# Kernel optimization log

Measured on AMD Instinct MI355X. Metric: run time of the kernel, lower is better.

Reference implementation:

```python
import jax, jax.numpy as jnp
import numpy as np
import math

N_NODES, CHANNELS, N_ELEM, N_FEAT = 4096, 128, 10, 128
LS_IN = [0, 1, 2]          # input irreps per channel: 0e+1o+2e -> dim 9
L_OUT = [0, 1]             # keep_irrep_out = {0e, 1o}
L12_MAX = 3                # cap on intermediate coupling
SLICES = {0: (0, 1), 1: (1, 4), 2: (4, 9)}
PATHS1 = [l for l in L_OUT if l in LS_IN]
PATHS2 = [(l1, l2, lo) for l1 in LS_IN for l2 in LS_IN for lo in L_OUT if abs(l1 - l2) <= lo <= l1 + l2]
T12_KEYS = [(l1, l2, l12) for l1 in LS_IN for l2 in LS_IN for l12 in range(abs(l1 - l2), min(l1 + l2, L12_MAX) + 1)]
PATHS3 = [(k, l3, lo) for k in T12_KEYS for l3 in LS_IN for lo in L_OUT if abs(k[2] - l3) <= lo <= k[2] + l3]

def _su2_cg(j1, m1, j2, m2, j3, m3):
    if m3 != m1 + m2:
        return 0.0
    f = math.factorial
    vmin = max(-j1 + j2 + m3, -j1 + m1, 0)
    vmax = min(j2 + j3 + m1, j3 - j1 + j2, j3 + m3)
    C = math.sqrt((2 * j3 + 1) * f(j3 + j1 - j2) * f(j3 - j1 + j2) * f(j1 + j2 - j3) * f(j3 + m3) * f(j3 - m3)
                  / (f(j1 + j2 + j3 + 1) * f(j1 - m1) * f(j1 + m1) * f(j2 - m2) * f(j2 + m2)))
    S = 0.0
    for v in range(vmin, vmax + 1):
        S += (-1) ** (v + j2 + m2) * f(j2 + j3 + m1 - v) * f(j1 - m1 + v) / (
            f(v) * f(j3 - j1 + j2 - v) * f(j3 + m3 - v) * f(v + j1 - j2 - m3))
    return C * S

def _c2r(l):
    # change of basis real -> complex spherical harmonics (e3nn convention)
    q = np.zeros((2 * l + 1, 2 * l + 1), dtype=np.complex128)
    for m in range(-l, 0):
        q[l + m, l + abs(m)] = 1.0 / math.sqrt(2)
        q[l + m, l - abs(m)] = -1j / math.sqrt(2)
    q[l, l] = 1.0
    for m in range(1, l + 1):
        q[l + m, l + abs(m)] = (-1) ** m / math.sqrt(2)
        q[l + m, l - abs(m)] = 1j * (-1) ** m / math.sqrt(2)
    return (-1j) ** l * q

_CG = {}
def real_cg(l1, l2, l3):
    key = (l1, l2, l3)
    if key not in _CG:
        Cc = np.zeros((2 * l1 + 1, 2 * l2 + 1, 2 * l3 + 1), dtype=np.complex128)
        for i, m1 in enumerate(range(-l1, l1 + 1)):
            for j, m2 in enumerate(range(-l2, l2 + 1)):
                for k, m3 in enumerate(range(-l3, l3 + 1)):
                    Cc[i, j, k] = _su2_cg(l1, m1, l2, m2, l3, m3)
        R = np.einsum('ij,kl,mn,ikn->jlm', _c2r(l1), _c2r(l2), np.conj(_c2r(l3).T), Cc)
        _CG[key] = np.real(R).astype(np.float32)
    return _CG[key]

def setup_inputs():
    key = jax.random.key(0)
    k = jax.random.split(key, 8)
    node_feats = jax.random.normal(k[0], (N_NODES, CHANNELS, 9), dtype=jnp.float32)
    species = jax.random.randint(k[1], (N_NODES,), 0, N_ELEM)
    w1 = jax.random.normal(k[2], (N_ELEM, len(PATHS1), CHANNELS), dtype=jnp.float32) / math.sqrt(len(PATHS1))
    w2 = jax.random.normal(k[3], (N_ELEM, len(PATHS2), CHANNELS), dtype=jnp.float32) / math.sqrt(len(PATHS2))
    w3 = jax.random.normal(k[4], (N_ELEM, len(PATHS3), CHANNELS), dtype=jnp.float32) / math.sqrt(len(PATHS3))
    lin_w0 = jax.random.normal(k[5], (CHANNELS, N_FEAT), dtype=jnp.float32)
    lin_w1 = jax.random.normal(k[6], (CHANNELS, N_FEAT), dtype=jnp.float32)
    return {"node_feats": node_feats, "w1": w1, "w2": w2, "w3": w3,
            "lin_w0": lin_w0, "lin_w1": lin_w1, "species": species}

def reference(node_feats, w1, w2, w3, lin_w0, lin_w1, species):
    n, c = node_feats.shape[:2]
    attrs = jax.nn.one_hot(species, N_ELEM, dtype=node_feats.dtype)
    A = {l: node_feats[..., SLICES[l][0]:SLICES[l][1]] for l in LS_IN}
    # element-dependent path weights per node
    w1n = jnp.einsum('ne,epc->npc', attrs, w1)
    w2n = jnp.einsum('ne,epc->npc', attrs, w2)
    w3n = jnp.einsum('ne,epc->npc', attrs, w3)
    B = {lo: jnp.zeros((n, c, 2 * lo + 1), node_feats.dtype) for lo in L_OUT}
    # correlation order 1
    for p, lo in enumerate(PATHS1):
        B[lo] = B[lo] + w1n[:, p, :, None] * A[lo]
    for p, (l1, l2, lo) in enumerate(PATHS2):
        cg = jnp.asarray(real_cg(l1, l2, lo))
        t = jnp.einsum('ijk,nci,ncj->nck', cg, A[l1], A[l2])
        B[lo] = B[lo] + w2n[:, p, :, None] * t
    T12 = {}
    for kk in T12_KEYS:
        l1, l2, l12 = kk
        T12[kk] = jnp.einsum('ijk,nci,ncj->nck', jnp.asarray(real_cg(l1, l2, l12)), A[l1], A[l2])
    for p, (kk, l3, lo) in enumerate(PATHS3):
        cg = jnp.asarray(real_cg(kk[2], l3, lo))
        t = jnp.einsum('ijk,nci,ncj->nck', cg, T12[kk], A[l3])
        B[lo] = B[lo] + w3n[:, p, :, None] * t
    # equivariant Linear: mix channel axis into num_features per output irrep
    s = 1.0 / math.sqrt(c)
    out0 = jnp.einsum('ncm,cf->nfm', B[0], lin_w0) * s
    out1 = jnp.einsum('ncm,cf->nfm', B[1], lin_w1) * s
    return jnp.concatenate([out0, out1], axis=-1)  # [N, F, 1+3]
```

## Files before the change

### kernel.cpp

```cpp
#include <hip/hip_runtime.h>
#include <utility>


#define NN 4096
#define NC 128
#define NE 10
#define LTN 8

typedef float v2f __attribute__((ext_vector_type(2)));

__device__ __forceinline__ v2f ld2(const float* p) {
  return *reinterpret_cast<const v2f*>(p);
}
__device__ __forceinline__ v2f cfma(float c, v2f x, v2f a) {
  v2f cc = {c, c};
  return __builtin_elementwise_fma(cc, x, a);
}
__device__ __forceinline__ v2f vfma(v2f w, v2f x, v2f a) {
  return __builtin_elementwise_fma(w, x, a);
}

template<typename F, int... Is>
__device__ __forceinline__ void sfor_impl(F&& f, std::integer_sequence<int, Is...>) {
  (f(std::integral_constant<int, Is>{}), ...);
}
template<int N, typename F>
__device__ __forceinline__ void sfor(F&& f) {
  sfor_impl((F&&)f, std::make_integer_sequence<int, N>{});
}

constexpr int T_L1c[19]  = {0,0,0,1,1,1,1,1,1,1,2,2,2,2,2,2,2,2,3};
constexpr int T_L2c[19]  = {0,1,2,0,1,1,1,2,2,2,0,1,1,1,2,2,2,2,2};
constexpr int T_L3c[19]  = {0,1,2,1,0,1,2,1,2,3,2,1,2,3,0,1,2,3,1};
constexpr int T_OFFc[19] = {0,1,10,35,44,53,80,125,170,245,350,375,420,495,600,625,700,825,1000};
constexpr int AOFFc[3]   = {0,1,4};

constexpr int P2U_L1c[7]  = {0,0,1,1,1,2,2};
constexpr int P2U_L2c[7]  = {0,1,1,1,2,2,2};
constexpr int P2U_LOc[7]  = {0,1,0,1,1,0,1};
constexpr int P2U_TBLc[7] = {0,1,4,5,7,14,15};
constexpr int P2U_WAc[7]  = {0,1,3,4,5,7,8};
constexpr int P2U_WBc[7]  = {-1,2,-1,-1,6,-1,-1};

constexpr int K_L1c[18]  = {0,0,0,1,1,1,1,1,1,1,2,2,2,2,2,2,2,2};
constexpr int K_L2c[18]  = {0,1,2,0,1,1,1,2,2,2,0,1,1,1,2,2,2,2};
constexpr int K_L12c[18] = {0,1,2,1,0,1,2,1,2,3,2,1,2,3,0,1,2,3};

constexpr int   TT_CANONc[18] = {0,1,2,1,4,5,6,7,8,9,2,7,8,9,14,15,16,17};
constexpr float TT_SGNc[18]   = {1,1,1,1,1,1,1,1,1,1,1,1,-1,1,1,1,1,1};
constexpr int CANONc[13] = {0,1,2,4,5,6,7,8,9,14,15,16,17};
constexpr int CONS2c[13] = {-1,3,10,-1,-1,-1,11,12,13,-1,-1,-1,-1};

constexpr int P3_STARTc[19] = {0,2,6,9,13,15,19,22,26,29,30,33,37,40,41,43,47,50,51};
constexpr int P3_L3c[51] = {
  0,1,  0,1,1,2,  1,2,2,  0,1,1,2,  0,1,  0,1,1,2,  1,2,2,  0,1,1,2,  1,2,2,
  2,  1,2,2,  0,1,1,2,  1,2,2,  2,  0,1,  0,1,1,2,  1,2,2,  2 };
constexpr int P3_LOc[51] = {
  0,1,  1,0,1,1,  1,0,1,  1,0,1,1,  0,1,  1,0,1,1,  1,0,1,  1,0,1,1,  1,0,1,
  1,  1,0,1,  1,0,1,1,  1,0,1,  1,  0,1,  1,0,1,1,  1,0,1,  1 };
constexpr int P3_TBLc[51] = {
  0,1,  3,4,5,7,  11,14,15,  3,4,5,7,  0,1,  3,4,5,7,  11,14,15,  3,4,5,7,
  11,14,15,  18,  11,14,15,  3,4,5,7,  11,14,15,  18,  0,1,  3,4,5,7,
  11,14,15,  18 };

constexpr double cfact(int n) { double r = 1.0; for (int i = 2; i <= n; ++i) r *= i; return r; }
constexpr double csqrt(double x) {
  if (x <= 0.0) return 0.0;
  double r = x > 1.0 ? x : 1.0;
  for (int i = 0; i < 64; ++i) r = 0.5 * (r + x / r);
  return r;
}
constexpr double su2cg(int j1, int m1, int j2, int m2, int j3, int m3) {
  if (m3 != m1 + m2) return 0.0;
  int vmin = -j1 + j2 + m3; if (-j1 + m1 > vmin) vmin = -j1 + m1; if (vmin < 0) vmin = 0;
  int vmax = j2 + j3 + m1; if (j3 - j1 + j2 < vmax) vmax = j3 - j1 + j2; if (j3 + m3 < vmax) vmax = j3 + m3;
  double C = csqrt((2.0 * j3 + 1.0)
                   * cfact(j3 + j1 - j2) * cfact(j3 - j1 + j2) * cfact(j1 + j2 - j3)
                   * cfact(j3 + m3) * cfact(j3 - m3)
                   / (cfact(j1 + j2 + j3 + 1) * cfact(j1 - m1) * cfact(j1 + m1)
                      * cfact(j2 - m2) * cfact(j2 + m2)));
  double S = 0.0;
  for (int v = vmin; v <= vmax; ++v) {
    double sgn = ((v + j2 + m2) & 1) ? -1.0 : 1.0;
    S += sgn * cfact(j2 + j3 + m1 - v) * cfact(j1 - m1 + v)
         / (cfact(v) * cfact(j3 - j1 + j2 - v) * cfact(j3 + m3 - v) * cfact(v + j1 - j2 - m3));
  }
  return C * S;
}

struct Cx { double re, im; };
constexpr Cx cxmul(Cx a, Cx b) { return Cx{a.re * b.re - a.im * b.im, a.re * b.im + a.im * b.re}; }
struct Row { int cnt; int col[2]; Cx v[2]; };

constexpr Row c2r_row(int l, int r) {
  Row out{0, {0, 0}, {{0, 0}, {0, 0}}};
  constexpr double is2 = 0.70710678118654752440;
  const int m = r - l;
  if (m < 0) {
    out.cnt = 2;
    out.col[0] = l - m; out.v[0] = Cx{is2, 0.0};
    out.col[1] = l + m; out.v[1] = Cx{0.0, -is2};
  } else if (m == 0) {
    out.cnt = 1; out.col[0] = l; out.v[0] = Cx{1.0, 0.0};
  } else {
    const double sgn = (m & 1) ? -1.0 : 1.0;
    out.cnt = 2;
    out.col[0] = l + m; out.v[0] = Cx{sgn * is2, 0.0};
    out.col[1] = l - m; out.v[1] = Cx{0.0, sgn * is2};
  }
  const int ph = l & 3;
  for (int a = 0; a < out.cnt; ++a) {
    Cx v = out.v[a];
    out.v[a] = (ph == 0) ? v
             : (ph == 1) ? Cx{v.im, -v.re}
             : (ph == 2) ? Cx{-v.re, -v.im}
                         : Cx{-v.im, v.re};
  }
  return out;
}

struct CGAll { float v[1105]; };
constexpr CGAll make_cg() {
  CGAll R{};
  for (int t = 0; t < 19; ++t) {
    const int l1 = T_L1c[t], l2 = T_L2c[t], l3 = T_L3c[t], off = T_OFFc[t];
    const int d1 = 2 * l1 + 1, d2 = 2 * l2 + 1, d3 = 2 * l3 + 1;
    double tmp[175] = {};
    for (int i = 0; i < d1; ++i) {
      const int m1 = i - l1;
      const Row r1 = c2r_row(l1, i);
      for (int k = 0; k < d2; ++k) {
        const int m2 = k - l2, m3 = m1 + m2;
        if (m3 < -l3 || m3 > l3) continue;
        const double cc = su2cg(l1, m1, l2, m2, l3, m3);
        if (cc == 0.0) continue;
        const Row r2 = c2r_row(l2, k);
        const Row r3 = c2r_row(l3, m3 + l3);
        for (int a = 0; a < r1.cnt; ++a)
          for (int b = 0; b < r2.cnt; ++b) {
            const Cx q12 = cxmul(r1.v[a], r2.v[b]);
            for (int cdx = 0; cdx < r3.cnt; ++cdx) {
              const double re = q12.re * r3.v[cdx].re + q12.im * r3.v[cdx].im;
              tmp[(r1.col[a] * d2 + r2.col[b]) * d3 + r3.col[cdx]] += re * cc;
            }
          }
      }
    }
    const int sz = d1 * d2 * d3;
    for (int e = 0; e < sz; ++e) R.v[off + e] = (float)tmp[e];
  }
  return R;
}
constexpr CGAll CG_ALL = make_cg();

constexpr bool check_cg_sym() {
  for (int t = 0; t < 18; ++t) {
    const int tc = TT_CANONc[t];
    if (tc == t) continue;
    const int l1 = K_L1c[t], l2 = K_L2c[t], l12 = K_L12c[t];
    const int d1 = 2*l1+1, d2 = 2*l2+1, d12 = 2*l12+1;
    for (int i = 0; i < d1; ++i)
      for (int j = 0; j < d2; ++j)
        for (int k = 0; k < d12; ++k) {
          float a = CG_ALL.v[T_OFFc[t]  + (i*d2 + j)*d12 + k];
          float b = TT_SGNc[t] * CG_ALL.v[T_OFFc[tc] + (j*d1 + i)*d12 + k];
          float d = a - b; if (d < 0) d = -d;
          if (d > 1e-5f) return false;
        }
  }
  return true;
}
static_assert(check_cg_sym(), "CG exchange symmetry violated");

__global__ __launch_bounds__(256) void epb_basis(
    const float* __restrict__ nf,
    const float* __restrict__ w1,
    const float* __restrict__ w2,
    const float* __restrict__ w3,
    const int*   __restrict__ species,
    float4* __restrict__ Bws)
{
  const int t  = threadIdx.x;
  const int nb = blockIdx.x * 4;
  const int nl = t >> 6;
  const int c0 = (t & 63) * 2;
  const int n  = nb + nl;
  const int s  = species[n];

  const float* ap = nf + ((size_t)n * NC + c0) * 9;
  v2f A[9];
  sfor<9>([&](auto I) { A[I.value] = v2f{ap[I.value], ap[I.value + 9]}; });

  const float* w1p = w1 + (size_t)s * 2  * NC + c0;
  const float* w2p = w2 + (size_t)s * 9  * NC + c0;
  const float* w3p = w3 + (size_t)s * 51 * NC + c0;

  v2f B[4];
  {
    const v2f wa = ld2(w1p), wb = ld2(w1p + NC);
    B[0] = wa * A[0];
    B[1] = wb * A[1];
    B[2] = wb * A[2];
    B[3] = wb * A[3];
  }

  sfor<7>([&](auto P) {
    constexpr int p  = P.value;
    constexpr int l1 = P2U_L1c[p], l2 = P2U_L2c[p], lo = P2U_LOc[p];
    constexpr int d1 = 2*l1+1, d2 = 2*l2+1, dl = 2*lo+1;
    constexpr int off = T_OFFc[P2U_TBLc[p]];
    v2f w = ld2(w2p + P2U_WAc[p] * NC);
    if constexpr (P2U_WBc[p] >= 0) w = w + ld2(w2p + P2U_WBc[p] * NC);
    sfor<dl>([&](auto Kk) {
      constexpr int k = Kk.value;
      v2f v = {0.f, 0.f};
      sfor<d1>([&](auto I) {
        sfor<d2>([&](auto J) {
          constexpr float cgc = CG_ALL.v[off + (I.value * d2 + J.value) * dl + k];
          if constexpr (cgc != 0.0f) {
            constexpr int ia = AOFFc[l1] + I.value, ja = AOFFc[l2] + J.value;
            constexpr int x = ia < ja ? ia : ja, y = ia < ja ? ja : ia;
            v = cfma(cgc, A[x] * A[y], v);
          }
        });
      });
      B[lo + k] = vfma(w, v, B[lo + k]);
    });
  });

  sfor<13>([&](auto CI) {
    constexpr int tk  = CANONc[CI.value];
    constexpr int l1  = K_L1c[tk], l2 = K_L2c[tk], l12 = K_L12c[tk];
    constexpr int d1  = 2*l1+1, d2 = 2*l2+1, d12 = 2*l12+1;
    constexpr int off = T_OFFc[tk];
    v2f tt[d12];
    sfor<d12>([&](auto Kk) {
      constexpr int k = Kk.value;
      v2f v = {0.f, 0.f};
      sfor<d1>([&](auto I) {
        sfor<d2>([&](auto J) {
          constexpr float cgc = CG_ALL.v[off + (I.value * d2 + J.value) * d12 + k];
          if constexpr (cgc != 0.0f) {
            constexpr int ia = AOFFc[l1] + I.value, ja = AOFFc[l2] + J.value;
            constexpr int x = ia < ja ? ia : ja, y = ia < ja ? ja : ia;
            v = cfma(cgc, A[x] * A[y], v);
          }
        });
      });
      tt[k] = v;
    });

    auto consume = [&](auto TK, auto SG) {
      constexpr int tkey = TK.value;
      constexpr float sgn = (float)SG.value;
      constexpr int pcnt = P3_STARTc[tkey + 1] - P3_STARTc[tkey];
      sfor<pcnt>([&](auto PP) {
        constexpr int p  = P3_STARTc[tkey] + PP.value;
        constexpr int l3 = P3_L3c[p], lo = P3_LOc[p];
        constexpr int d3 = 2*l3+1, dl = 2*lo+1;
        constexpr int off2 = T_OFFc[P3_TBLc[p]];
        const v2f w = ld2(w3p + p * NC);
        sfor<dl>([&](auto M) {
          v2f v = {0.f, 0.f};
          sfor<d12>([&](auto Kk) {
            sfor<d3>([&](auto J) {
              constexpr float cgc = sgn * CG_ALL.v[off2 + (Kk.value * d3 + J.value) * dl + M.value];
              if constexpr (cgc != 0.0f)
                v = cfma(cgc, tt[Kk.value] * A[AOFFc[l3] + J.value], v);
            });
          });
          B[lo + M.value] = vfma(w, v, B[lo + M.value]);
        });
      });
    };
    consume(std::integral_constant<int, tk>{}, std::integral_constant<int, 1>{});
    constexpr int td = CONS2c[CI.value];
    if constexpr (td >= 0)
      consume(std::integral_constant<int, td>{},
              std::integral_constant<int, (int)TT_SGNc[td]>{});
  });

  Bws[(size_t)n * NC + c0]     = make_float4(B[0].x, B[1].x, B[2].x, B[3].x);
  Bws[(size_t)n * NC + c0 + 1] = make_float4(B[0].y, B[1].y, B[2].y, B[3].y);
}

__global__ __launch_bounds__(256) void epb_linear(
    const float4* __restrict__ Bws,
    const float4* __restrict__ lw0_4,
    const float4* __restrict__ lw1_4,
    float* __restrict__ out)
{
  __shared__ float4 W0[64 * 32];
  __shared__ float4 W1[64 * 32];
  __shared__ float4 Bsh[LTN * NC];
  const int t  = threadIdx.x;
  const int nb = blockIdx.x * LTN;

  {
    const float4* src = Bws + (size_t)nb * NC;
    sfor<4>([&](auto I) { Bsh[t + 256 * I.value] = src[t + 256 * I.value]; });
  }

  const int q  = t & 31;
  const int nl = t >> 5;

  float4 o0{0,0,0,0}, o1{0,0,0,0}, o2{0,0,0,0}, o3{0,0,0,0};

  #pragma unroll 1
  for (int ph = 0; ph < 2; ++ph) {
    __syncthreads();
    {
      const float4* s0 = lw0_4 + ph * (64 * 32);
      const float4* s1 = lw1_4 + ph * (64 * 32);
      sfor<8>([&](auto I) { W0[t + 256 * I.value] = s0[t + 256 * I.value]; });
      sfor<8>([&](auto I) { W1[t + 256 * I.value] = s1[t + 256 * I.value]; });
    }
    __syncthreads();

    const float4* bp = &Bsh[nl * NC + ph * 64];
    #pragma unroll 4
    for (int ch = 0; ch < 64; ++ch) {
      const float4 wa = W0[ch * 32 + q];
      const float4 wb = W1[ch * 32 + q];
      const float4 b  = bp[ch];
      o0.x = fmaf(b.x, wa.x, o0.x); o0.y = fmaf(b.y, wb.x, o0.y);
      o0.z = fmaf(b.z, wb.x, o0.z); o0.w = fmaf(b.w, wb.x, o0.w);
      o1.x = fmaf(b.x, wa.y, o1.x); o1.y = fmaf(b.y, wb.y, o1.y);
      o1.z = fmaf(b.z, wb.y, o1.z); o1.w = fmaf(b.w, wb.y, o1.w);
      o2.x = fmaf(b.x, wa.z, o2.x); o2.y = fmaf(b.y, wb.z, o2.y);
      o2.z = fmaf(b.z, wb.z, o2.z); o2.w = fmaf(b.w, wb.z, o2.w);
      o3.x = fmaf(b.x, wa.w, o3.x); o3.y = fmaf(b.y, wb.w, o3.y);
      o3.z = fmaf(b.z, wb.w, o3.z); o3.w = fmaf(b.w, wb.w, o3.w);
    }
  }

  const float s4 = 0.08838834764831845f;
  float4* o4 = reinterpret_cast<float4*>(out) + (size_t)(nb + nl) * NC + 4 * q;
  o4[0] = make_float4(o0.x*s4, o0.y*s4, o0.z*s4, o0.w*s4);
  o4[1] = make_float4(o1.x*s4, o1.y*s4, o1.z*s4, o1.w*s4);
  o4[2] = make_float4(o2.x*s4, o2.y*s4, o2.z*s4, o2.w*s4);
  o4[3] = make_float4(o3.x*s4, o3.y*s4, o3.z*s4, o3.w*s4);
}

extern "C" void kernel_launch(void* const* d_in, const int* in_sizes, int n_in,
                              void* d_out, int out_size, void* d_ws, size_t ws_size,
                              hipStream_t stream) {
  const float* nf  = (const float*)d_in[0];
  const float* w1  = (const float*)d_in[1];
  const float* w2  = (const float*)d_in[2];
  const float* w3  = (const float*)d_in[3];
  const float* lw0 = (const float*)d_in[4];
  const float* lw1 = (const float*)d_in[5];
  const int*   spc = (const int*)  d_in[6];
  float* out = (float*)d_out;
  float4* Bws = (float4*)d_ws;
  (void)ws_size; (void)in_sizes; (void)n_in; (void)out_size;

  hipLaunchKernelGGL(epb_basis, dim3(NN / 4), dim3(256), 0, stream,
                     nf, w1, w2, w3, spc, Bws);
  hipLaunchKernelGGL(epb_linear, dim3(NN / LTN), dim3(256), 0, stream,
                     Bws, (const float4*)lw0, (const float4*)lw1, out);
}
```

Baseline: 103.5 us.

## Fuse basis and linear kernels into one with in-block split-K reduction

Merges the basis computation and the channel-mixing linear into one kernel, so B stays in shared memory instead of going through a global workspace, and one launch is removed. The linear stage now reads weights straight from global/L2 rather than staging them in LDS. Each wave handles a 32-channel slice for two nodes, and partial sums are reduced through shared memory. The trade-offs are more LDS per block, only 4 nodes per block sharing each weight read, and higher register pressure in the combined kernel.

Result: faster. 100.1 us (-3.3%).

```diff
diff --git a/kernel.cpp b/kernel.cpp
--- a/kernel.cpp
+++ b/kernel.cpp
@@ -5,7 +5,6 @@
 #define NN 4096
 #define NC 128
 #define NE 10
-#define LTN 8
 
 typedef float v2f __attribute__((ext_vector_type(2)));
 
@@ -172,174 +171,184 @@
 }
 static_assert(check_cg_sym(), "CG exchange symmetry violated");
 
-__global__ __launch_bounds__(256) void epb_basis(
-    const float* __restrict__ nf,
-    const float* __restrict__ w1,
-    const float* __restrict__ w2,
-    const float* __restrict__ w3,
-    const int*   __restrict__ species,
-    float4* __restrict__ Bws)
+__global__ __launch_bounds__(256) void epb_fused(
+    const float*  __restrict__ nf,
+    const float*  __restrict__ w1,
+    const float*  __restrict__ w2,
+    const float*  __restrict__ w3,
+    const float4* __restrict__ lw0_4,
+    const float4* __restrict__ lw1_4,
+    const int*    __restrict__ species,
+    float* __restrict__ out)
 {
+  __shared__ float4 Bsh[4 * NC];
+  __shared__ float4 Red[16 * NC];
+
   const int t  = threadIdx.x;
   const int nb = blockIdx.x * 4;
-  const int nl = t >> 6;
-  const int c0 = (t & 63) * 2;
-  const int n  = nb + nl;
-  const int s  = species[n];
-
-  const float* ap = nf + ((size_t)n * NC + c0) * 9;
-  v2f A[9];
-  sfor<9>([&](auto I) { A[I.value] = v2f{ap[I.value], ap[I.value + 9]}; });
-
-  const float* w1p = w1 + (size_t)s * 2  * NC + c0;
-  const float* w2p = w2 + (size_t)s * 9  * NC + c0;
-  const float* w3p = w3 + (size_t)s * 51 * NC + c0;
-
-  v2f B[4];
+
   {
-    const v2f wa = ld2(w1p), wb = ld2(w1p + NC);
-    B[0] = wa * A[0];
-    B[1] = wb * A[1];
-    B[2] = wb * A[2];
-    B[3] = wb * A[3];
-  }
-
-  sfor<7>([&](auto P) {
-    constexpr int p  = P.value;
-    constexpr int l1 = P2U_L1c[p], l2 = P2U_L2c[p], lo = P2U_LOc[p];
-    constexpr int d1 = 2*l1+1, d2 = 2*l2+1, dl = 2*lo+1;
-    constexpr int off = T_OFFc[P2U_TBLc[p]];
-    v2f w = ld2(w2p + P2U_WAc[p] * NC);
-    if constexpr (P2U_WBc[p] >= 0) w = w + ld2(w2p + P2U_WBc[p] * NC);
-    sfor<dl>([&](auto Kk) {
-      constexpr int k = Kk.value;
-      v2f v = {0.f, 0.f};
-      sfor<d1>([&](auto I) {
-        sfor<d2>([&](auto J) {
-          constexpr float cgc = CG_ALL.v[off + (I.value * d2 + J.value) * dl + k];
-          if constexpr (cgc != 0.0f) {
-            constexpr int ia = AOFFc[l1] + I.value, ja = AOFFc[l2] + J.value;
-            constexpr int x = ia < ja ? ia : ja, y = ia < ja ? ja : ia;
-            v = cfma(cgc, A[x] * A[y], v);
-          }
+    const int nl = t >> 6;
+    const int c0 = (t & 63) * 2;
+    const int n  = nb + nl;
+    const int s  = species[n];
+
+    const float* ap = nf + ((size_t)n * NC + c0) * 9;
+    v2f A[9];
+    sfor<9>([&](auto I) { A[I.value] = v2f{ap[I.value], ap[I.value + 9]}; });
+
+    const float* w1p = w1 + (size_t)s * 2  * NC + c0;
+    const float* w2p = w2 + (size_t)s * 9  * NC + c0;
+    const float* w3p = w3 + (size_t)s * 51 * NC + c0;
+
+    v2f B[4];
+    {
+      const v2f wa = ld2(w1p), wb = ld2(w1p + NC);
+      B[0] = wa * A[0];
+      B[1] = wb * A[1];
+      B[2] = wb * A[2];
+      B[3] = wb * A[3];
+    }
+
+    sfor<7>([&](auto P) {
+      constexpr int p  = P.value;
+      constexpr int l1 = P2U_L1c[p], l2 = P2U_L2c[p], lo = P2U_LOc[p];
+      constexpr int d1 = 2*l1+1, d2 = 2*l2+1, dl = 2*lo+1;
+      constexpr int off = T_OFFc[P2U_TBLc[p]];
+      v2f w = ld2(w2p + P2U_WAc[p] * NC);
+      if constexpr (P2U_WBc[p] >= 0) w = w + ld2(w2p + P2U_WBc[p] * NC);
+      sfor<dl>([&](auto Kk) {
+        constexpr int k = Kk.value;
+        v2f v = {0.f, 0.f};
+        sfor<d1>([&](auto I) {
+          sfor<d2>([&](auto J) {
+            constexpr float cgc = CG_ALL.v[off + (I.value * d2 + J.value) * dl + k];
+            if constexpr (cgc != 0.0f) {
+              constexpr int ia = AOFFc[l1] + I.value, ja = AOFFc[l2] + J.value;
+              constexpr int x = ia < ja ? ia : ja, y = ia < ja ? ja : ia;
+              v = cfma(cgc, A[x] * A[y], v);
+            }
+          });
         });
+        B[lo + k] = vfma(w, v, B[lo + k]);
       });
-      B[lo + k] = vfma(w, v, B[lo + k]);
+    });
+
+    sfor<13>([&](auto CI) {
+      constexpr int tk  = CANONc[CI.value];
+      constexpr int l1  = K_L1c[tk], l2 = K_L2c[tk], l12 = K_L12c[tk];
+      constexpr int d1  = 2*l1+1, d2 = 2*l2+1, d12 = 2*l12+1;
+      constexpr int off = T_OFFc[tk];
+      v2f tt[d12];
+      sfor<d12>([&](auto Kk) {
+        constexpr int k = Kk.value;
+        v2f v = {0.f, 0.f};
+        sfor<d1>([&](auto I) {
+          sfor<d2>([&](auto J) {
+            constexpr float cgc = CG_ALL.v[off + (I.value * d2 + J.value) * d12 + k];
+            if constexpr (cgc != 0.0f) {
+              constexpr int ia = AOFFc[l1] + I.value, ja = AOFFc[l2] + J.value;
+              constexpr int x = ia < ja ? ia : ja, y = ia < ja ? ja : ia;
+              v = cfma(cgc, A[x] * A[y], v);
+            }
+          });
+        });
+        tt[k] = v;
+      });
+
+      auto consume = [&](auto TK, auto SG) {
+        constexpr int tkey = TK.value;
+        constexpr float sgn = (float)SG.value;
+        constexpr int pcnt = P3_STARTc[tkey + 1] - P3_STARTc[tkey];
+        sfor<pcnt>([&](auto PP) {
+          constexpr int p  = P3_STARTc[tkey] + PP.value;
+          constexpr int l3 = P3_L3c[p], lo = P3_LOc[p];
+          constexpr int d3 = 2*l3+1, dl = 2*lo+1;
+          constexpr int off2 = T_OFFc[P3_TBLc[p]];
+          const v2f w = ld2(w3p + p * NC);
+          sfor<dl>([&](auto M) {
+            v2f v = {0.f, 0.f};
+            sfor<d12>([&](auto Kk) {
+              sfor<d3>([&](auto J) {
+                constexpr float cgc = sgn * CG_ALL.v[off2 + (Kk.value * d3 + J.value) * dl + M.value];
+                if constexpr (cgc != 0.0f)
+                  v = cfma(cgc, tt[Kk.value] * A[AOFFc[l3] + J.value], v);
+              });
+            });
+            B[lo + M.value] = vfma(w, v, B[lo + M.value]);
+          });
+        });
+      };
+      consume(std::integral_constant<int, tk>{}, std::integral_constant<int, 1>{});
+      constexpr int td = CONS2c[CI.value];
+      if constexpr (td >= 0)
+        consume(std::integral_constant<int, td>{},
+                std::integral_constant<int, (int)TT_SGNc[td]>{});
+    });
+
+    Bsh[nl * NC + c0]     = make_float4(B[0].x, B[1].x, B[2].x, B[3].x);
+    Bsh[nl * NC + c0 + 1] = make_float4(B[0].y, B[1].y, B[2].y, B[3].y);
+  }
+  __syncthreads();
+
+  const int q   = t & 31;
+  const int dup = (t >> 5) & 1;
+  const int wv  = t >> 6;
+  const int n0  = dup * 2;
+
+  float4 acc[2][4] = {};
+
+  const float4* w0c = lw0_4 + (size_t)(wv * 32) * 32 + q;
+  const float4* w1c = lw1_4 + (size_t)(wv * 32) * 32 + q;
+  const float4* bp0 = &Bsh[ n0      * NC + wv * 32];
+  const float4* bp1 = &Bsh[(n0 + 1) * NC + wv * 32];
+
+  #pragma unroll 8
+  for (int i = 0; i < 32; ++i) {
+    const float4 wa = w0c[i * 32];
+    const float4 wb = w1c[i * 32];
+    const float4 ba = bp0[i];
+    const float4 bb = bp1[i];
+#define FQ(f, waf, wbf) \
+    acc[0][f].x = fmaf(ba.x, waf, acc[0][f].x); \
+    acc[0][f].y = fmaf(ba.y, wbf, acc[0][f].y); \
+    acc[0][f].z = fmaf(ba.z, wbf, acc[0][f].z); \
+    acc[0][f].w = fmaf(ba.w, wbf, acc[0][f].w); \
+    acc[1][f].x = fmaf(bb.x, waf, acc[1][f].x); \
+    acc[1][f].y = fmaf(bb.y, wbf, acc[1][f].y); \
+    acc[1][f].z = fmaf(bb.z, wbf, acc[1][f].z); \
+    acc[1][f].w = fmaf(bb.w, wbf, acc[1][f].w);
+    FQ(0, wa.x, wb.x)
+    FQ(1, wa.y, wb.y)
+    FQ(2, wa.z, wb.z)
+    FQ(3, wa.w, wb.w)
+#undef FQ
+  }
+
+  sfor<2>([&](auto NN_) {
+    sfor<4>([&](auto F_) {
+      Red[((n0 + NN_.value) * 4 + F_.value) * NC + wv * 32 + q] = acc[NN_.value][F_.value];
     });
   });
-
-  sfor<13>([&](auto CI) {
-    constexpr int tk  = CANONc[CI.value];
-    constexpr int l1  = K_L1c[tk], l2 = K_L2c[tk], l12 = K_L12c[tk];
-    constexpr int d1  = 2*l1+1, d2 = 2*l2+1, d12 = 2*l12+1;
-    constexpr int off = T_OFFc[tk];
-    v2f tt[d12];
-    sfor<d12>([&](auto Kk) {
-      constexpr int k = Kk.value;
-      v2f v = {0.f, 0.f};
-      sfor<d1>([&](auto I) {
-        sfor<d2>([&](auto J) {
-          constexpr float cgc = CG_ALL.v[off + (I.value * d2 + J.value) * d12 + k];
-          if constexpr (cgc != 0.0f) {
-            constexpr int ia = AOFFc[l1] + I.value, ja = AOFFc[l2] + J.value;
-            constexpr int x = ia < ja ? ia : ja, y = ia < ja ? ja : ia;
-            v = cfma(cgc, A[x] * A[y], v);
-          }
-        });
-      });
-      tt[k] = v;
-    });
-
-    auto consume = [&](auto TK, auto SG) {
-      constexpr int tkey = TK.value;
-      constexpr float sgn = (float)SG.value;
-      constexpr int pcnt = P3_STARTc[tkey + 1] - P3_STARTc[tkey];
-      sfor<pcnt>([&](auto PP) {
-        constexpr int p  = P3_STARTc[tkey] + PP.value;
-        constexpr int l3 = P3_L3c[p], lo = P3_LOc[p];
-        constexpr int d3 = 2*l3+1, dl = 2*lo+1;
-        constexpr int off2 = T_OFFc[P3_TBLc[p]];
-        const v2f w = ld2(w3p + p * NC);
-        sfor<dl>([&](auto M) {
-          v2f v = {0.f, 0.f};
-          sfor<d12>([&](auto Kk) {
-            sfor<d3>([&](auto J) {
-              constexpr float cgc = sgn * CG_ALL.v[off2 + (Kk.value * d3 + J.value) * dl + M.value];
-              if constexpr (cgc != 0.0f)
-                v = cfma(cgc, tt[Kk.value] * A[AOFFc[l3] + J.value], v);
-            });
-          });
-          B[lo + M.value] = vfma(w, v, B[lo + M.value]);
-        });
-      });
-    };
-    consume(std::integral_constant<int, tk>{}, std::integral_constant<int, 1>{});
-    constexpr int td = CONS2c[CI.value];
-    if constexpr (td >= 0)
-      consume(std::integral_constant<int, td>{},
-              std::integral_constant<int, (int)TT_SGNc[td]>{});
+  __syncthreads();
+
+  const float s4 = 0.08838834764831845f;
+  float4* o4 = reinterpret_cast<float4*>(out);
+  sfor<2>([&](auto O_) {
+    const int oid = 2 * t + O_.value;
+    const int n   = oid >> 7;
+    const int rem = oid & 127;
+    const int row = (n * 4 + (rem & 3)) * NC + (rem >> 2);
+    const float4 r0 = Red[row];
+    const float4 r1 = Red[row + 32];
+    const float4 r2 = Red[row + 64];
+    const float4 r3 = Red[row + 96];
+    o4[(size_t)(nb + n) * NC + rem] = make_float4(
+        ((r0.x + r1.x) + (r2.x + r3.x)) * s4,
+        ((r0.y + r1.y) + (r2.y + r3.y)) * s4,
+        ((r0.z + r1.z) + (r2.z + r3.z)) * s4,
+        ((r0.w + r1.w) + (r2.w + r3.w)) * s4);
   });
-
-  Bws[(size_t)n * NC + c0]     = make_float4(B[0].x, B[1].x, B[2].x, B[3].x);
-  Bws[(size_t)n * NC + c0 + 1] = make_float4(B[0].y, B[1].y, B[2].y, B[3].y);
-}
-
-__global__ __launch_bounds__(256) void epb_linear(
-    const float4* __restrict__ Bws,
-    const float4* __restrict__ lw0_4,
-    const float4* __restrict__ lw1_4,
-    float* __restrict__ out)
-{
-  __shared__ float4 W0[64 * 32];
-  __shared__ float4 W1[64 * 32];
-  __shared__ float4 Bsh[LTN * NC];
-  const int t  = threadIdx.x;
-  const int nb = blockIdx.x * LTN;
-
-  {
-    const float4* src = Bws + (size_t)nb * NC;
-    sfor<4>([&](auto I) { Bsh[t + 256 * I.value] = src[t + 256 * I.value]; });
-  }
-
-  const int q  = t & 31;
-  const int nl = t >> 5;
-
-  float4 o0{0,0,0,0}, o1{0,0,0,0}, o2{0,0,0,0}, o3{0,0,0,0};
-
-  #pragma unroll 1
-  for (int ph = 0; ph < 2; ++ph) {
-    __syncthreads();
-    {
-      const float4* s0 = lw0_4 + ph * (64 * 32);
-      const float4* s1 = lw1_4 + ph * (64 * 32);
-      sfor<8>([&](auto I) { W0[t + 256 * I.value] = s0[t + 256 * I.value]; });
-      sfor<8>([&](auto I) { W1[t + 256 * I.value] = s1[t + 256 * I.value]; });
-    }
-    __syncthreads();
-
-    const float4* bp = &Bsh[nl * NC + ph * 64];
-    #pragma unroll 4
-    for (int ch = 0; ch < 64; ++ch) {
-      const float4 wa = W0[ch * 32 + q];
-      const float4 wb = W1[ch * 32 + q];
-      const float4 b  = bp[ch];
-      o0.x = fmaf(b.x, wa.x, o0.x); o0.y = fmaf(b.y, wb.x, o0.y);
-      o0.z = fmaf(b.z, wb.x, o0.z); o0.w = fmaf(b.w, wb.x, o0.w);
-      o1.x = fmaf(b.x, wa.y, o1.x); o1.y = fmaf(b.y, wb.y, o1.y);
-      o1.z = fmaf(b.z, wb.y, o1.z); o1.w = fmaf(b.w, wb.y, o1.w);
-      o2.x = fmaf(b.x, wa.z, o2.x); o2.y = fmaf(b.y, wb.z, o2.y);
-      o2.z = fmaf(b.z, wb.z, o2.z); o2.w = fmaf(b.w, wb.z, o2.w);
-      o3.x = fmaf(b.x, wa.w, o3.x); o3.y = fmaf(b.y, wb.w, o3.y);
-      o3.z = fmaf(b.z, wb.w, o3.z); o3.w = fmaf(b.w, wb.w, o3.w);
-    }
-  }
-
-  const float s4 = 0.08838834764831845f;
-  float4* o4 = reinterpret_cast<float4*>(out) + (size_t)(nb + nl) * NC + 4 * q;
-  o4[0] = make_float4(o0.x*s4, o0.y*s4, o0.z*s4, o0.w*s4);
-  o4[1] = make_float4(o1.x*s4, o1.y*s4, o1.z*s4, o1.w*s4);
-  o4[2] = make_float4(o2.x*s4, o2.y*s4, o2.z*s4, o2.w*s4);
-  o4[3] = make_float4(o3.x*s4, o3.y*s4, o3.z*s4, o3.w*s4);
 }
 
 extern "C" void kernel_launch(void* const* d_in, const int* in_sizes, int n_in,
@@ -353,11 +362,9 @@
   const float* lw1 = (const float*)d_in[5];
   const int*   spc = (const int*)  d_in[6];
   float* out = (float*)d_out;
-  float4* Bws = (float4*)d_ws;
-  (void)ws_size; (void)in_sizes; (void)n_in; (void)out_size;
-
-  hipLaunchKernelGGL(epb_basis, dim3(NN / 4), dim3(256), 0, stream,
-                     nf, w1, w2, w3, spc, Bws);
-  hipLaunchKernelGGL(epb_linear, dim3(NN / LTN), dim3(256), 0, stream,
-                     Bws, (const float4*)lw0, (const float4*)lw1, out);
-}
+  (void)d_ws; (void)ws_size; (void)in_sizes; (void)n_in; (void)out_size;
+
+  hipLaunchKernelGGL(epb_fused, dim3(NN / 4), dim3(256), 0, stream,
+                     nf, w1, w2, w3, (const float4*)lw0, (const float4*)lw1,
+                     spc, out);
+}
```

## Restructure linear kernel to read weights from global with split-K reduction

Applied to the files above, without the earlier changes.

The linear stage no longer stages the full weight matrices and B rows in shared memory. Each block now handles 16 nodes and a quarter of the output features, and splits the channel dimension across two thread halves that are combined through a small shared-memory reduction. This removes the large per-block LDS staging and its barriers and raises block count. In exchange, weight and B reads go straight to global/L2 with strided access and less reuse per block.

Result: slower. 134.5 us (+30.0%).

```diff
diff --git a/kernel.cpp b/kernel.cpp
--- a/kernel.cpp
+++ b/kernel.cpp
@@ -5,7 +5,6 @@
 #define NN 4096
 #define NC 128
 #define NE 10
-#define LTN 8
 
 typedef float v2f __attribute__((ext_vector_type(2)));
 
@@ -290,56 +289,53 @@
     const float4* __restrict__ lw1_4,
     float* __restrict__ out)
 {
-  __shared__ float4 W0[64 * 32];
-  __shared__ float4 W1[64 * 32];
-  __shared__ float4 Bsh[LTN * NC];
   const int t  = threadIdx.x;
-  const int nb = blockIdx.x * LTN;
-
-  {
-    const float4* src = Bws + (size_t)nb * NC;
-    sfor<4>([&](auto I) { Bsh[t + 256 * I.value] = src[t + 256 * I.value]; });
-  }
-
-  const int q  = t & 31;
-  const int nl = t >> 5;
-
-  float4 o0{0,0,0,0}, o1{0,0,0,0}, o2{0,0,0,0}, o3{0,0,0,0};
-
-  #pragma unroll 1
-  for (int ph = 0; ph < 2; ++ph) {
-    __syncthreads();
-    {
-      const float4* s0 = lw0_4 + ph * (64 * 32);
-      const float4* s1 = lw1_4 + ph * (64 * 32);
-      sfor<8>([&](auto I) { W0[t + 256 * I.value] = s0[t + 256 * I.value]; });
-      sfor<8>([&](auto I) { W1[t + 256 * I.value] = s1[t + 256 * I.value]; });
-    }
-    __syncthreads();
-
-    const float4* bp = &Bsh[nl * NC + ph * 64];
-    #pragma unroll 4
-    for (int ch = 0; ch < 64; ++ch) {
-      const float4 wa = W0[ch * 32 + q];
-      const float4 wb = W1[ch * 32 + q];
-      const float4 b  = bp[ch];
-      o0.x = fmaf(b.x, wa.x, o0.x); o0.y = fmaf(b.y, wb.x, o0.y);
-      o0.z = fmaf(b.z, wb.x, o0.z); o0.w = fmaf(b.w, wb.x, o0.w);
-      o1.x = fmaf(b.x, wa.y, o1.x); o1.y = fmaf(b.y, wb.y, o1.y);
-      o1.z = fmaf(b.z, wb.y, o1.z); o1.w = fmaf(b.w, wb.y, o1.w);
-      o2.x = fmaf(b.x, wa.z, o2.x); o2.y = fmaf(b.y, wb.z, o2.y);
-      o2.z = fmaf(b.z, wb.z, o2.z); o2.w = fmaf(b.w, wb.z, o2.w);
-      o3.x = fmaf(b.x, wa.w, o3.x); o3.y = fmaf(b.y, wb.w, o3.y);
-      o3.z = fmaf(b.z, wb.w, o3.z); o3.w = fmaf(b.w, wb.w, o3.w);
-    }
-  }
-
-  const float s4 = 0.08838834764831845f;
-  float4* o4 = reinterpret_cast<float4*>(out) + (size_t)(nb + nl) * NC + 4 * q;
-  o4[0] = make_float4(o0.x*s4, o0.y*s4, o0.z*s4, o0.w*s4);
-  o4[1] = make_float4(o1.x*s4, o1.y*s4, o1.z*s4, o1.w*s4);
-  o4[2] = make_float4(o2.x*s4, o2.y*s4, o2.z*s4, o2.w*s4);
-  o4[3] = make_float4(o3.x*s4, o3.y*s4, o3.z*s4, o3.w*s4);
+  const int fc = blockIdx.x & 3;
+  const int nb = (blockIdx.x >> 2) * 16;
+
+  const int nl = t & 15;
+  const int fq = (t >> 4) & 7;
+  const int h  = t >> 7;
+
+  const int n  = nb + nl;
+  const int fquad = fc * 8 + fq;
+
+  const float4* bp  = Bws + (size_t)n * NC + h * 64;
+  const float4* w0c = lw0_4 + (size_t)(h * 64) * 32 + fquad;
+  const float4* w1c = lw1_4 + (size_t)(h * 64) * 32 + fquad;
+
+  float4 acc[4] = {};
+
+  #pragma unroll 4
+  for (int i = 0; i < 64; ++i) {
+    const float4 b  = bp[i];
+    const float4 wa = w0c[i * 32];
+    const float4 wb = w1c[i * 32];
+    acc[0].x = fmaf(b.x, wa.x, acc[0].x); acc[0].y = fmaf(b.y, wb.x, acc[0].y);
+    acc[0].z = fmaf(b.z, wb.x, acc[0].z); acc[0].w = fmaf(b.w, wb.x, acc[0].w);
+    acc[1].x = fmaf(b.x, wa.y, acc[1].x); acc[1].y = fmaf(b.y, wb.y, acc[1].y);
+    acc[1].z = fmaf(b.z, wb.y, acc[1].z); acc[1].w = fmaf(b.w, wb.y, acc[1].w);
+    acc[2].x = fmaf(b.x, wa.z, acc[2].x); acc[2].y = fmaf(b.y, wb.z, acc[2].y);
+    acc[2].z = fmaf(b.z, wb.z, acc[2].z); acc[2].w = fmaf(b.w, wb.z, acc[2].w);
+    acc[3].x = fmaf(b.x, wa.w, acc[3].x); acc[3].y = fmaf(b.y, wb.w, acc[3].y);
+    acc[3].z = fmaf(b.z, wb.w, acc[3].z); acc[3].w = fmaf(b.w, wb.w, acc[3].w);
+  }
+
+  __shared__ float4 Red[256 * 4];
+  sfor<4>([&](auto F_) { Red[(t & 127) * 4 + F_.value + (t >> 7) * 512] = acc[F_.value]; });
+  __syncthreads();
+  if (h == 0) {
+    const float s4 = 0.08838834764831845f;
+    float4* o4 = reinterpret_cast<float4*>(out);
+    sfor<4>([&](auto F_) {
+      constexpr int f = F_.value;
+      const float4 a = acc[f];
+      const float4 c2 = Red[(t & 127) * 4 + f + 512];
+      o4[(size_t)n * NC + fquad * 4 + f] = make_float4(
+          (a.x + c2.x) * s4, (a.y + c2.y) * s4,
+          (a.z + c2.z) * s4, (a.w + c2.w) * s4);
+    });
+  }
 }
 
 extern "C" void kernel_launch(void* const* d_in, const int* in_sizes, int n_in,
@@ -358,6 +354,6 @@
 
   hipLaunchKernelGGL(epb_basis, dim3(NN / 4), dim3(256), 0, stream,
                      nf, w1, w2, w3, spc, Bws);
-  hipLaunchKernelGGL(epb_linear, dim3(NN / LTN), dim3(256), 0, stream,
+  hipLaunchKernelGGL(epb_linear, dim3(NN / 16 * 4), dim3(256), 0, stream,
                      Bws, (const float4*)lw0, (const float4*)lw1, out);
 }
```
